# Performance work log

Hardware: AMD Instinct MI355X
Metric: run time of the kernel (lower is better)

Reference implementation:

```python
import jax, jax.numpy as jnp
import numpy as np

N_EMBED = 8192
EMBED_DIM = 64
BETA = 0.25


def setup_inputs() -> dict:
    key = jax.random.key(0)
    k_z, k_e = jax.random.split(key)
    z = jax.random.normal(k_z, (16, 4096, EMBED_DIM), dtype=jnp.float32)
    # embedding.weight.data.uniform_(-1/n_embed, 1/n_embed)
    embedding = jax.random.uniform(
        k_e, (N_EMBED, EMBED_DIM), dtype=jnp.float32,
        minval=-1.0 / N_EMBED, maxval=1.0 / N_EMBED)
    return {"z": z, "embedding": embedding}


def reference(z, embedding):
    # z: [B, H, C] with C == embed_dim (no permute needed)
    B, H, C = z.shape
    z_flat = z.reshape(-1, C)                      # [N, C]
    # squared euclidean distances: ||z||^2 + ||e||^2 - 2 z e^T
    d = (jnp.sum(z_flat ** 2, axis=1, keepdims=True)
         + jnp.sum(embedding ** 2, axis=1)
         - 2.0 * jnp.matmul(z_flat, embedding.T))  # [N, n_embed]
    idx = jnp.argmin(d, axis=1)                    # [N]
    z_q = embedding[idx].reshape(z.shape)          # gather + reshape
    sg = jax.lax.stop_gradient
    loss = (jnp.mean((sg(z_q) - z) ** 2)
            + BETA * jnp.mean((z_q - sg(z)) ** 2))
    # straight-through estimator
    z_q = z + sg(z_q - z)
    return z_q, loss, idx.reshape(B, H)
```

## Files before the change

kernel.cpp:

```cpp
#include <hip/hip_runtime.h>

typedef __attribute__((ext_vector_type(8))) short short8;
typedef __attribute__((ext_vector_type(16))) float floatx16;
typedef unsigned int u32;
typedef unsigned short u16;
typedef unsigned long long u64;

#define NROWS 65536
#define NEMB 8192
#define DIM 64
#define LOSS_OFF ((size_t)NROWS * DIM)
#define IDX_OFF (LOSS_OFF + 1)
#define CAPQ 16
#define CSTRIDE 66
#define NPREST 4

#define WS_EFRAG_OFF 0u
#define WS_BEST_OFF  (1u << 20)
#define WS_QUEUE_OFF ((1u << 20) + (512u << 10))
#define WS_LPART_OFF (WS_QUEUE_OFF + (512u << 10))
#define WS_QCNT_OFF  (WS_LPART_OFF + 8192u)
#define WS_NEED      (WS_QCNT_OFF + 64u)

__device__ __forceinline__ unsigned short f2bf(float f) {
    u32 x = __float_as_uint(f);
    return (unsigned short)((x + 0x7fffu + ((x >> 16) & 1u)) >> 16);
}

__device__ __forceinline__ float zsum_np(const float* zf) {
    float r[8];
#pragma unroll
    for (int j = 0; j < 8; ++j) r[j] = zf[j] * zf[j];
#pragma unroll
    for (int i = 8; i < 64; i += 8) {
#pragma unroll
        for (int j = 0; j < 8; ++j) r[j] += zf[i + j] * zf[i + j];
    }
    return ((r[0] + r[1]) + (r[2] + r[3])) + ((r[4] + r[5]) + (r[6] + r[7]));
}

__device__ __forceinline__ float dot_chain(const float* zf, const float* e) {
    float acc = 0.f;
#pragma unroll
    for (int i = 0; i < 16; ++i) {
        float4 ev = ((const float4*)e)[i];
        acc = fmaf(zf[4 * i + 0], ev.x, acc);
        acc = fmaf(zf[4 * i + 1], ev.y, acc);
        acc = fmaf(zf[4 * i + 2], ev.z, acc);
        acc = fmaf(zf[4 * i + 3], ev.w, acc);
    }
    return acc;
}

__device__ __forceinline__ float vmax16_3(const floatx16& a) {
    float m0 = fmaxf(fmaxf(a[0], a[1]), a[2]);
    float m1 = fmaxf(fmaxf(a[3], a[4]), a[5]);
    float m2 = fmaxf(fmaxf(a[6], a[7]), a[8]);
    float m3 = fmaxf(fmaxf(a[9], a[10]), a[11]);
    float m4 = fmaxf(fmaxf(a[12], a[13]), a[14]);
    float n0 = fmaxf(fmaxf(m0, m1), m2);
    float n1 = fmaxf(fmaxf(m3, m4), a[15]);
    return fmaxf(n0, n1);
}

__device__ __forceinline__ float fmax_h32(float x) {
#if defined(__has_builtin)
#if __has_builtin(__builtin_amdgcn_permlane32_swap)
    typedef __attribute__((ext_vector_type(2))) unsigned int uint2v;
    uint2v r = __builtin_amdgcn_permlane32_swap(
        __float_as_uint(x), __float_as_uint(x), false, false);
    return fmaxf(__uint_as_float(r[0]), __uint_as_float(r[1]));
#else
    return fmaxf(x, __shfl_xor(x, 32));
#endif
#else
    return fmaxf(x, __shfl_xor(x, 32));
#endif
}

extern "C" __global__ __launch_bounds__(256)
void vq_prep(const float* __restrict__ emb, u32* __restrict__ efrag,
             u64* __restrict__ best, u32* __restrict__ qcount) {
    int tid = blockIdx.x * 256 + threadIdx.x;
    int t = tid >> 8, kc = (tid >> 5) & 7, m = tid & 31;
    const float* e = emb + (((size_t)t * 32 + m) * 64 + kc * 8);
    float4 a = ((const float4*)e)[0];
    float4 b = ((const float4*)e)[1];
    u32 w0 = (u32)f2bf(a.x) | ((u32)f2bf(a.y) << 16);
    u32 w1 = (u32)f2bf(a.z) | ((u32)f2bf(a.w) << 16);
    u32 w2 = (u32)f2bf(b.x) | ((u32)f2bf(b.y) << 16);
    u32 w3 = (u32)f2bf(b.z) | ((u32)f2bf(b.w) << 16);
    ((uint4*)efrag)[tid] = make_uint4(w0, w1, w2, w3);
    best[tid] = ~0ull;
    if (tid < 16) qcount[tid] = 0u;
}

extern "C" __global__ __launch_bounds__(256, 4)
void vq_screen(const float* __restrict__ z, const u32* __restrict__ efrag,
               const float* __restrict__ emb, u64* __restrict__ best,
               u32* __restrict__ queue, u32* __restrict__ qcount) {
    __shared__ u16 cand[128 * CSTRIDE];
    __shared__ u32 cnt_l[512];
    __shared__ float runm_sh[128][2];
    const int tid = threadIdx.x;
    const int wave = tid >> 6, lane = tid & 63;
    const int rlo = lane & 31, h = lane >> 5;
    const int rowblk = blockIdx.x >> 1, halfid = blockIdx.x & 1;
    const int rowbase = rowblk * 128 + (wave >> 1) * 64;
    const int sub = (wave & 1) * 2 + h;
    const int wp = wave & 1;
    const int rowl0 = (wave >> 1) * 64 + rlo;
    const int rowl1 = rowl0 + 32;
    const int ebh = halfid * 4096 + wp * 64 + 4 * h;

    if (tid < 128) { runm_sh[tid][0] = -3.4e38f; runm_sh[tid][1] = -3.4e38f; }

    const u32* fb = efrag + (u32)halfid * 131072u
                  + (u32)(wp * 2048 + h * 128 + rlo * 4);

    short8 zfr[2][4];
    float eps_[2];
#pragma unroll
    for (int rt = 0; rt < 2; ++rt) {
        const float* zp = z + (size_t)(rowbase + rt * 32 + rlo) * 64;
        float sa = 0.f;
#pragma unroll
        for (int s = 0; s < 4; ++s) {
            const float4* p = (const float4*)(zp + s * 16 + h * 8);
            float4 a = p[0], b = p[1];
            union { short8 v; unsigned short e[8]; } u;
            u.e[0] = f2bf(a.x); u.e[1] = f2bf(a.y);
            u.e[2] = f2bf(a.z); u.e[3] = f2bf(a.w);
            u.e[4] = f2bf(b.x); u.e[5] = f2bf(b.y);
            u.e[6] = f2bf(b.z); u.e[7] = f2bf(b.w);
            zfr[rt][s] = u.v;
            sa += fabsf(a.x) + fabsf(a.y) + fabsf(a.z) + fabsf(a.w)
                + fabsf(b.x) + fabsf(b.y) + fabsf(b.z) + fabsf(b.w);
        }
        sa += __shfl_xor(sa, 32);
        eps_[rt] = fmaf(1.1e-6f, sa, 1e-7f);
    }
    float runm[2] = { -3.4e38f, -3.4e38f };
    u32 pc[2] = { 0u, 0u };
    const u32 cb0 = (u32)rowl0 * CSTRIDE + (u32)sub * CAPQ;
    const u32 cb1 = (u32)rowl1 * CSTRIDE + (u32)sub * CAPQ;
    const floatx16 ZACC = 0.f;

    __syncthreads();

#define PF(B_, T_, E_) do { \
    const u32* bp_ = fb + ((u32)(T_) * 4096u + (u32)(E_) * 1024u); \
    B_[0] = *(const short8*)(bp_); \
    B_[1] = *(const short8*)(bp_ + 256); \
    B_[2] = *(const short8*)(bp_ + 512); \
    B_[3] = *(const short8*)(bp_ + 768); \
} while (0)

#define TILE(B_, RT_, T_, EE_, SCAN_, CB_) do { \
    floatx16 a_ = __builtin_amdgcn_mfma_f32_32x32x16_bf16(B_[0], zfr[RT_][0], ZACC, 0, 0, 0); \
    a_ = __builtin_amdgcn_mfma_f32_32x32x16_bf16(B_[1], zfr[RT_][1], a_, 0, 0, 0); \
    a_ = __builtin_amdgcn_mfma_f32_32x32x16_bf16(B_[2], zfr[RT_][2], a_, 0, 0, 0); \
    a_ = __builtin_amdgcn_mfma_f32_32x32x16_bf16(B_[3], zfr[RT_][3], a_, 0, 0, 0); \
    float vm_ = vmax16_3(a_); \
    runm[RT_] = fmax_h32(fmaxf(runm[RT_], vm_)); \
    if (SCAN_) { \
        const float thr_ = runm[RT_] - eps_[RT_]; \
        if (vm_ >= thr_) { \
            const int ebj_ = ebh + (T_) * 128 + (EE_) * 32; \
            _Pragma("unroll") \
            for (int r_ = 0; r_ < 16; ++r_) { \
                if (a_[r_] >= thr_) { \
                    int j_ = ebj_ + ((r_ & 3) + 8 * (r_ >> 2)); \
                    if (pc[RT_] < CAPQ) cand[CB_ + pc[RT_]] = (u16)j_; \
                    pc[RT_]++;                     \
                } \
            } \
        } \
    } \
} while (0)

#define SUBSTAGE(B_, T_, EE_, SCAN_) do { \
    if (EE_ == 0) {                                \
        runm[0] = fmaxf(runm[0], runm_sh[rowl0][wp ^ 1]); \
        runm[1] = fmaxf(runm[1], runm_sh[rowl1][wp ^ 1]); \
    } \
    TILE(B_, 0, T_, EE_, SCAN_, cb0); \
    TILE(B_, 1, T_, EE_, SCAN_, cb1); \
    if (EE_ == 1 && h == 0) {                      \
        runm_sh[rowl0][wp] = runm[0]; \
        runm_sh[rowl1][wp] = runm[1]; \
    } \
} while (0)

    {
        short8 b0[4], b1[4];
        PF(b0, 0, 0);
        for (int t = 0; t < NPREST; ++t) {
            PF(b1, t, 1);
            SUBSTAGE(b0, t, 0, false);
            PF(b0, (t == NPREST - 1) ? 0 : (t + 1), 0);
            SUBSTAGE(b1, t, 1, false);
        }
        for (int t = 0; t < 32; ++t) {
            PF(b1, t, 1);
            SUBSTAGE(b0, t, 0, true);
            PF(b0, (t == 31) ? 31 : (t + 1), 0);
            SUBSTAGE(b1, t, 1, true);
        }
    }
#undef SUBSTAGE
#undef TILE
#undef PF

    cnt_l[(rowl0 << 2) + sub] = pc[0];
    cnt_l[(rowl1 << 2) + sub] = pc[1];
    __syncthreads();

    {
        const int rl = lane & 31, half = lane >> 5;
        const int rowl = wave * 32 + rl;
        const int grow = rowblk * 128 + rowl;
        const u32 ca = cnt_l[(rowl << 2) + 2 * half];
        const u32 cb = cnt_l[(rowl << 2) + 2 * half + 1];
        u32 ovf = (u32)((ca > CAPQ) | (cb > CAPQ));
        ovf |= (u32)__shfl_xor((int)ovf, 32);

        if (!ovf) {
            float zf[64];
            const float4* zp = (const float4*)(z + (size_t)grow * 64);
#pragma unroll
            for (int i = 0; i < 16; ++i) {
                float4 a = zp[i];
                zf[4 * i + 0] = a.x; zf[4 * i + 1] = a.y;
                zf[4 * i + 2] = a.z; zf[4 * i + 3] = a.w;
            }
            const float zs = zsum_np(zf);
            u64 b = ~0ull;
            const u32 cbase = (u32)rowl * CSTRIDE + (u32)(2 * half) * CAPQ;
            for (u32 s = 0; s < ca; ++s) {
                u32 j = (u32)cand[cbase + s];
                float d = fmaf(-2.f, dot_chain(zf, emb + (size_t)j * 64), zs);
                u64 p = ((u64)__float_as_uint(d) << 32) | (u64)j;
                b = p < b ? p : b;
            }
            for (u32 s = 0; s < cb; ++s) {
                u32 j = (u32)cand[cbase + CAPQ + s];
                float d = fmaf(-2.f, dot_chain(zf, emb + (size_t)j * 64), zs);
                u64 p = ((u64)__float_as_uint(d) << 32) | (u64)j;
                b = p < b ? p : b;
            }
            u64 o = __shfl_xor(b, 32);
            b = o < b ? o : b;
            if (half == 0) atomicMin(&best[grow], b);
        } else if (half == 0) {
            u32 pos = atomicAdd(qcount, 1u);
            queue[pos] = (u32)grow | ((u32)halfid << 16);
        }
    }
}

extern "C" __global__ __launch_bounds__(256)
void vq_final(const float* __restrict__ z, const float* __restrict__ emb,
              u64* __restrict__ best, const u32* __restrict__ queue,
              const u32* __restrict__ qcount, float* __restrict__ out,
              float* __restrict__ lpart) {
    __shared__ float lsum[4];
    __shared__ u64 red[4];
    const int tid = threadIdx.x, wave = tid >> 6, lane = tid & 63;

    u32 n = qcount[0]; if (n > 2u * (u32)NROWS) n = 2u * (u32)NROWS;
    for (u32 qi = 0; qi < n; ++qi) {
        const u32 e = queue[qi];
        const int row = (int)(e & 0xFFFFu);
        if ((row >> 7) != (int)blockIdx.x) continue;
        const int hb = (int)((e >> 16) & 1u) * 4096;
        const float4* zp = (const float4*)(z + (size_t)row * 64);
        float zf[64];
#pragma unroll
        for (int i = 0; i < 16; ++i) {
            float4 a = zp[i];
            zf[4 * i + 0] = a.x; zf[4 * i + 1] = a.y;
            zf[4 * i + 2] = a.z; zf[4 * i + 3] = a.w;
        }
        const float zs = zsum_np(zf);
        u64 b = ~0ull;
#pragma unroll 2
        for (int j = tid; j < 4096; j += 256) {
            const int gj = hb + j;
            float d = fmaf(-2.f, dot_chain(zf, emb + (size_t)gj * 64), zs);
            u64 p = ((u64)__float_as_uint(d) << 32) | (u64)gj;
            b = p < b ? p : b;
        }
#pragma unroll
        for (int off = 32; off; off >>= 1) {
            u64 o = __shfl_xor(b, off);
            b = o < b ? o : b;
        }
        if (lane == 0) red[wave] = b;
        __syncthreads();
        if (tid == 0) {
            u64 bb = red[0];
#pragma unroll
            for (int w = 1; w < 4; ++w) { u64 o = red[w]; bb = o < bb ? o : bb; }
            atomicMin(&best[row], bb);
        }
        __syncthreads();
    }
    __syncthreads();

    const int r2 = tid >> 1, hf = tid & 1;
    const int grow = blockIdx.x * 128 + r2;
    const u32 wj = (u32)best[grow];
    if (hf == 0) out[IDX_OFF + grow] = (float)wj;
    float lp = 0.f;
    {
        const float4* ep = (const float4*)(emb + (size_t)wj * 64) + hf * 8;
        const float4* zp4 = (const float4*)(z + (size_t)grow * 64) + hf * 8;
        float4* oq = (float4*)(out + (size_t)grow * 64) + hf * 8;
#pragma unroll
        for (int i = 0; i < 8; ++i) {
            float4 ev = ep[i];
            float4 zv = zp4[i];
            oq[i] = ev;
            float dx = ev.x - zv.x, dy = ev.y - zv.y;
            float dzv = ev.z - zv.z, dw = ev.w - zv.w;
            lp = fmaf(dx, dx, fmaf(dy, dy, fmaf(dzv, dzv, fmaf(dw, dw, lp))));
        }
    }
#pragma unroll
    for (int off = 32; off; off >>= 1) lp += __shfl_down(lp, off);
    if (lane == 0) lsum[wave] = lp;
    __syncthreads();
    if (tid == 0)
        lpart[blockIdx.x] = (lsum[0] + lsum[1]) + (lsum[2] + lsum[3]);
}

extern "C" __global__ __launch_bounds__(256)
void vq_lossred(const float* __restrict__ lpart, float* __restrict__ out) {
    __shared__ float s[256];
    const int tid = threadIdx.x;
    float v = 0.f;
    for (int i = tid; i < 512; i += 256) v += lpart[i];
    s[tid] = v; __syncthreads();
    for (int off = 128; off; off >>= 1) {
        if (tid < off) s[tid] += s[tid + off];
        __syncthreads();
    }
    if (tid == 0) out[LOSS_OFF] = 1.25f * s[0] / 4194304.f;
}

extern "C" __global__ __launch_bounds__(256, 2)
void vq_legacy(const float* __restrict__ z, const float* __restrict__ emb,
               float* __restrict__ out, float* __restrict__ ws) {
    __shared__ float tile[128 * 64];
    __shared__ float red_d[4][128];
    __shared__ int   red_i[4][128];
    const int tid = threadIdx.x, lane = tid & 63, wave = tid >> 6;
    const int r0 = blockIdx.x * 128 + lane;
    float z0f[64], z1f[64];
    {
        const float4* p0 = (const float4*)(z + (size_t)r0 * 64);
        const float4* p1 = (const float4*)(z + ((size_t)r0 + 64) * 64);
#pragma unroll
        for (int i = 0; i < 16; ++i) {
            float4 a = p0[i];
            z0f[4*i+0]=a.x; z0f[4*i+1]=a.y; z0f[4*i+2]=a.z; z0f[4*i+3]=a.w;
            float4 b = p1[i];
            z1f[4*i+0]=b.x; z1f[4*i+1]=b.y; z1f[4*i+2]=b.z; z1f[4*i+3]=b.w;
        }
    }
    const float zs0 = zsum_np(z0f), zs1 = zsum_np(z1f);
    float bd0 = 3.402823466e38f, bd1 = 3.402823466e38f;
    int bi0 = 0, bi1 = 0;
    for (int t = 0; t < 64; ++t) {
        __syncthreads();
        {
            const float4* src = (const float4*)(emb + (size_t)t * 128 * 64);
            float4* dst = (float4*)tile;
#pragma unroll
            for (int i = 0; i < 8; ++i) dst[tid + i * 256] = src[tid + i * 256];
        }
        __syncthreads();
        const int base = wave * 32;
#pragma unroll 2
        for (int jg = 0; jg < 32; jg += 4) {
            const float* e = tile + (size_t)(base + jg) * 64;
            float a00=0,a10=0,a20=0,a30=0,a01=0,a11=0,a21=0,a31=0;
#pragma unroll
            for (int i = 0; i < 16; ++i) {
                float4 ea = ((const float4*)(e))[i];
                float4 eb = ((const float4*)(e + 64))[i];
                float4 ec = ((const float4*)(e + 128))[i];
                float4 ed = ((const float4*)(e + 192))[i];
                float x0=z0f[4*i],x1=z0f[4*i+1],x2=z0f[4*i+2],x3=z0f[4*i+3];
                float y0=z1f[4*i],y1=z1f[4*i+1],y2=z1f[4*i+2],y3=z1f[4*i+3];
                a00=fmaf(x0,ea.x,a00);a00=fmaf(x1,ea.y,a00);a00=fmaf(x2,ea.z,a00);a00=fmaf(x3,ea.w,a00);
                a10=fmaf(x0,eb.x,a10);a10=fmaf(x1,eb.y,a10);a10=fmaf(x2,eb.z,a10);a10=fmaf(x3,eb.w,a10);
                a20=fmaf(x0,ec.x,a20);a20=fmaf(x1,ec.y,a20);a20=fmaf(x2,ec.z,a20);a20=fmaf(x3,ec.w,a20);
                a30=fmaf(x0,ed.x,a30);a30=fmaf(x1,ed.y,a30);a30=fmaf(x2,ed.z,a30);a30=fmaf(x3,ed.w,a30);
                a01=fmaf(y0,ea.x,a01);a01=fmaf(y1,ea.y,a01);a01=fmaf(y2,ea.z,a01);a01=fmaf(y3,ea.w,a01);
                a11=fmaf(y0,eb.x,a11);a11=fmaf(y1,eb.y,a11);a11=fmaf(y2,eb.z,a11);a11=fmaf(y3,eb.w,a11);
                a21=fmaf(y0,ec.x,a21);a21=fmaf(y1,ec.y,a21);a21=fmaf(y2,ec.z,a21);a21=fmaf(y3,ec.w,a21);
                a31=fmaf(y0,ed.x,a31);a31=fmaf(y1,ed.y,a31);a31=fmaf(y2,ed.z,a31);a31=fmaf(y3,ed.w,a31);
            }
            const int gj = t * 128 + base + jg;
            float d;
            d=fmaf(-2.f,a00,zs0); if(d<bd0){bd0=d;bi0=gj;}
            d=fmaf(-2.f,a10,zs0); if(d<bd0){bd0=d;bi0=gj+1;}
            d=fmaf(-2.f,a20,zs0); if(d<bd0){bd0=d;bi0=gj+2;}
            d=fmaf(-2.f,a30,zs0); if(d<bd0){bd0=d;bi0=gj+3;}
            d=fmaf(-2.f,a01,zs1); if(d<bd1){bd1=d;bi1=gj;}
            d=fmaf(-2.f,a11,zs1); if(d<bd1){bd1=d;bi1=gj+1;}
            d=fmaf(-2.f,a21,zs1); if(d<bd1){bd1=d;bi1=gj+2;}
            d=fmaf(-2.f,a31,zs1); if(d<bd1){bd1=d;bi1=gj+3;}
        }
    }
    red_d[wave][lane]=bd0; red_i[wave][lane]=bi0;
    red_d[wave][lane+64]=bd1; red_i[wave][lane+64]=bi1;
    __syncthreads();
    if (wave == 0) {
        float blk = 0.f;
#pragma unroll
        for (int half = 0; half < 2; ++half) {
            const int lrow = lane + half * 64;
            const float* zrf = half ? z1f : z0f;
            float bd = red_d[0][lrow]; int bi = red_i[0][lrow];
#pragma unroll
            for (int w = 1; w < 4; ++w) {
                float dd = red_d[w][lrow]; int ii = red_i[w][lrow];
                if (dd < bd || (dd == bd && ii < bi)) { bd = dd; bi = ii; }
            }
            const size_t row = (size_t)blockIdx.x * 128 + lrow;
            out[IDX_OFF + row] = (float)bi;
            const float4* ep = (const float4*)(emb + (size_t)bi * 64);
            float4* oq = (float4*)(out + row * 64);
            float ls = 0.f;
#pragma unroll
            for (int i = 0; i < 16; ++i) {
                float4 ev = ep[i];
                oq[i] = ev;
                float dx=ev.x-zrf[4*i], dy=ev.y-zrf[4*i+1];
                float dzv=ev.z-zrf[4*i+2], dw=ev.w-zrf[4*i+3];
                ls=fmaf(dx,dx,ls); ls=fmaf(dy,dy,ls); ls=fmaf(dzv,dzv,ls); ls=fmaf(dw,dw,ls);
            }
            blk += ls;
        }
#pragma unroll
        for (int off = 32; off; off >>= 1) blk += __shfl_down(blk, off);
        if (lane == 0) ws[blockIdx.x] = blk;
    }
}

extern "C" __global__ __launch_bounds__(512)
void vq_legacy_loss(const float* __restrict__ ws, float* __restrict__ out) {
    __shared__ float s[8];
    const int tid = threadIdx.x;
    float v = ws[tid];
#pragma unroll
    for (int off = 32; off; off >>= 1) v += __shfl_down(v, off);
    if ((tid & 63) == 0) s[tid >> 6] = v;
    __syncthreads();
    if (tid == 0) {
        float t = 0.f;
#pragma unroll
        for (int i = 0; i < 8; ++i) t += s[i];
        out[LOSS_OFF] = 1.25f * t / 4194304.f;
    }
}

extern "C" void kernel_launch(void* const* d_in, const int* in_sizes, int n_in,
                              void* d_out, int out_size, void* d_ws, size_t ws_size,
                              hipStream_t stream) {
    const float* z   = (const float*)d_in[0];
    const float* emb = (const float*)d_in[1];
    float* out = (float*)d_out;
    if (ws_size < (size_t)WS_NEED) {
        float* ws = (float*)d_ws;
        vq_legacy<<<512, 256, 0, stream>>>(z, emb, out, ws);
        vq_legacy_loss<<<1, 512, 0, stream>>>(ws, out);
        return;
    }
    char* wsb = (char*)d_ws;
    u32* efrag   = (u32*)(wsb + WS_EFRAG_OFF);
    u64* best    = (u64*)(wsb + WS_BEST_OFF);
    u32* queue   = (u32*)(wsb + WS_QUEUE_OFF);
    float* lpart = (float*)(wsb + WS_LPART_OFF);
    u32* qcount  = (u32*)(wsb + WS_QCNT_OFF);
    vq_prep<<<256, 256, 0, stream>>>(emb, efrag, best, qcount);
    vq_screen<<<1024, 256, 0, stream>>>(z, efrag, emb, best, queue, qcount);
    vq_final<<<512, 256, 0, stream>>>(z, emb, best, queue, qcount, out, lpart);
    vq_lossred<<<1, 256, 0, stream>>>(lpart, out);
}
```

Measured before the change: 193.6 us.

## Fuse final rescan and loss reduction into screen kernel via last-block counters

Removes the vq_final and vq_lossred launches. The second of the two screen blocks to finish a row block now does the queued fallback rescans, the gather and output writes, and the per-block loss partial. A global counter then elects the last block to reduce the loss. This saves two kernel launches and lets tail work overlap with screening in other blocks. In exchange it adds atomics and fences, and the queued rescan is serialized inside the finishing block. The shared-memory footprint of vq_screen grows, which may affect occupancy.

```diff
diff --git a/kernel.cpp b/kernel.cpp
--- a/kernel.cpp
+++ b/kernel.cpp
@@ -20,7 +20,8 @@
 #define WS_QUEUE_OFF ((1u << 20) + (512u << 10))
 #define WS_LPART_OFF (WS_QUEUE_OFF + (512u << 10))
 #define WS_QCNT_OFF  (WS_LPART_OFF + 8192u)
-#define WS_NEED      (WS_QCNT_OFF + 64u)
+#define WS_DONE_OFF  (WS_QCNT_OFF + 64u)
+#define WS_NEED      (WS_DONE_OFF + 2112u)
 
 __device__ __forceinline__ unsigned short f2bf(float f) {
     u32 x = __float_as_uint(f);
@@ -80,7 +81,8 @@
 
 extern "C" __global__ __launch_bounds__(256)
 void vq_prep(const float* __restrict__ emb, u32* __restrict__ efrag,
-             u64* __restrict__ best, u32* __restrict__ qcount) {
+             u64* __restrict__ best, u32* __restrict__ qcount,
+             u32* __restrict__ done) {
     int tid = blockIdx.x * 256 + threadIdx.x;
     int t = tid >> 8, kc = (tid >> 5) & 7, m = tid & 31;
     const float* e = emb + (((size_t)t * 32 + m) * 64 + kc * 8);
@@ -93,15 +95,22 @@
     ((uint4*)efrag)[tid] = make_uint4(w0, w1, w2, w3);
     best[tid] = ~0ull;
     if (tid < 16) qcount[tid] = 0u;
+    if (tid < 513) done[tid] = 0u;
 }
 
 extern "C" __global__ __launch_bounds__(256, 4)
 void vq_screen(const float* __restrict__ z, const u32* __restrict__ efrag,
                const float* __restrict__ emb, u64* __restrict__ best,
-               u32* __restrict__ queue, u32* __restrict__ qcount) {
+               u32* __restrict__ queue, u32* __restrict__ qcount,
+               u32* __restrict__ done, float* __restrict__ out,
+               float* __restrict__ lpart) {
     __shared__ u16 cand[128 * CSTRIDE];
     __shared__ u32 cnt_l[512];
     __shared__ float runm_sh[128][2];
+    __shared__ u64 red[4];
+    __shared__ float lsum[4];
+    __shared__ float sred[256];
+    __shared__ u32 dold;
     const int tid = threadIdx.x;
     const int wave = tid >> 6, lane = tid & 63;
     const int rlo = lane & 31, h = lane >> 5;
@@ -257,96 +266,102 @@
             queue[pos] = (u32)grow | ((u32)halfid << 16);
         }
     }
-}
-
-extern "C" __global__ __launch_bounds__(256)
-void vq_final(const float* __restrict__ z, const float* __restrict__ emb,
-              u64* __restrict__ best, const u32* __restrict__ queue,
-              const u32* __restrict__ qcount, float* __restrict__ out,
-              float* __restrict__ lpart) {
-    __shared__ float lsum[4];
-    __shared__ u64 red[4];
-    const int tid = threadIdx.x, wave = tid >> 6, lane = tid & 63;
-
-    u32 n = qcount[0]; if (n > 2u * (u32)NROWS) n = 2u * (u32)NROWS;
-    for (u32 qi = 0; qi < n; ++qi) {
-        const u32 e = queue[qi];
-        const int row = (int)(e & 0xFFFFu);
-        if ((row >> 7) != (int)blockIdx.x) continue;
-        const int hb = (int)((e >> 16) & 1u) * 4096;
-        const float4* zp = (const float4*)(z + (size_t)row * 64);
-        float zf[64];
-#pragma unroll
-        for (int i = 0; i < 16; ++i) {
-            float4 a = zp[i];
-            zf[4 * i + 0] = a.x; zf[4 * i + 1] = a.y;
-            zf[4 * i + 2] = a.z; zf[4 * i + 3] = a.w;
-        }
-        const float zs = zsum_np(zf);
-        u64 b = ~0ull;
+
+    __threadfence();
+    __syncthreads();
+    if (tid == 0) dold = atomicAdd(&done[rowblk], 1u);
+    __syncthreads();
+    if (dold == 0) return;
+    __threadfence();
+
+    {
+        u32 n = atomicAdd(qcount, 0u);
+        if (n > 2u * (u32)NROWS) n = 2u * (u32)NROWS;
+        for (u32 qi = 0; qi < n; ++qi) {
+            const u32 e = atomicAdd(&queue[qi], 0u);
+            const int row = (int)(e & 0xFFFFu);
+            if ((row >> 7) != rowblk) continue;
+            const int hb = (int)((e >> 16) & 1u) * 4096;
+            const float4* zp = (const float4*)(z + (size_t)row * 64);
+            float zf[64];
+#pragma unroll
+            for (int i = 0; i < 16; ++i) {
+                float4 a = zp[i];
+                zf[4 * i + 0] = a.x; zf[4 * i + 1] = a.y;
+                zf[4 * i + 2] = a.z; zf[4 * i + 3] = a.w;
+            }
+            const float zs = zsum_np(zf);
+            u64 b = ~0ull;
 #pragma unroll 2
-        for (int j = tid; j < 4096; j += 256) {
-            const int gj = hb + j;
-            float d = fmaf(-2.f, dot_chain(zf, emb + (size_t)gj * 64), zs);
-            u64 p = ((u64)__float_as_uint(d) << 32) | (u64)gj;
-            b = p < b ? p : b;
-        }
-#pragma unroll
-        for (int off = 32; off; off >>= 1) {
-            u64 o = __shfl_xor(b, off);
-            b = o < b ? o : b;
-        }
-        if (lane == 0) red[wave] = b;
+            for (int j = tid; j < 4096; j += 256) {
+                const int gj = hb + j;
+                float d = fmaf(-2.f, dot_chain(zf, emb + (size_t)gj * 64), zs);
+                u64 p = ((u64)__float_as_uint(d) << 32) | (u64)gj;
+                b = p < b ? p : b;
+            }
+#pragma unroll
+            for (int off = 32; off; off >>= 1) {
+                u64 o = __shfl_xor(b, off);
+                b = o < b ? o : b;
+            }
+            if (lane == 0) red[wave] = b;
+            __syncthreads();
+            if (tid == 0) {
+                u64 bb = red[0];
+#pragma unroll
+                for (int w = 1; w < 4; ++w) { u64 o = red[w]; bb = o < bb ? o : bb; }
+                atomicMin(&best[row], bb);
+            }
+            __syncthreads();
+        }
+    }
+    __syncthreads();
+
+    {
+        const int r2 = tid >> 1, hf = tid & 1;
+        const int growE = rowblk * 128 + r2;
+        const u64 bjv = atomicAdd(&best[growE], 0ull);
+        const u32 wj = (u32)bjv;
+        if (hf == 0) out[IDX_OFF + growE] = (float)wj;
+        float lp = 0.f;
+        {
+            const float4* ep = (const float4*)(emb + (size_t)wj * 64) + hf * 8;
+            const float4* zp4 = (const float4*)(z + (size_t)growE * 64) + hf * 8;
+            float4* oq = (float4*)(out + (size_t)growE * 64) + hf * 8;
+#pragma unroll
+            for (int i = 0; i < 8; ++i) {
+                float4 ev = ep[i];
+                float4 zv = zp4[i];
+                oq[i] = ev;
+                float dx = ev.x - zv.x, dy = ev.y - zv.y;
+                float dzv = ev.z - zv.z, dw = ev.w - zv.w;
+                lp = fmaf(dx, dx, fmaf(dy, dy, fmaf(dzv, dzv, fmaf(dw, dw, lp))));
+            }
+        }
+#pragma unroll
+        for (int off = 32; off; off >>= 1) lp += __shfl_down(lp, off);
+        if (lane == 0) lsum[wave] = lp;
         __syncthreads();
         if (tid == 0) {
-            u64 bb = red[0];
-#pragma unroll
-            for (int w = 1; w < 4; ++w) { u64 o = red[w]; bb = o < bb ? o : bb; }
-            atomicMin(&best[row], bb);
+            lpart[rowblk] = (lsum[0] + lsum[1]) + (lsum[2] + lsum[3]);
+            __threadfence();
+            dold = atomicAdd(&done[512], 1u);
         }
         __syncthreads();
-    }
-    __syncthreads();
-
-    const int r2 = tid >> 1, hf = tid & 1;
-    const int grow = blockIdx.x * 128 + r2;
-    const u32 wj = (u32)best[grow];
-    if (hf == 0) out[IDX_OFF + grow] = (float)wj;
-    float lp = 0.f;
+        if (dold != 511) return;
+        __threadfence();
+    }
+
     {
-        const float4* ep = (const float4*)(emb + (size_t)wj * 64) + hf * 8;
-        const float4* zp4 = (const float4*)(z + (size_t)grow * 64) + hf * 8;
-        float4* oq = (float4*)(out + (size_t)grow * 64) + hf * 8;
-#pragma unroll
-        for (int i = 0; i < 8; ++i) {
-            float4 ev = ep[i];
-            float4 zv = zp4[i];
-            oq[i] = ev;
-            float dx = ev.x - zv.x, dy = ev.y - zv.y;
-            float dzv = ev.z - zv.z, dw = ev.w - zv.w;
-            lp = fmaf(dx, dx, fmaf(dy, dy, fmaf(dzv, dzv, fmaf(dw, dw, lp))));
-        }
-    }
-#pragma unroll
-    for (int off = 32; off; off >>= 1) lp += __shfl_down(lp, off);
-    if (lane == 0) lsum[wave] = lp;
-    __syncthreads();
-    if (tid == 0)
-        lpart[blockIdx.x] = (lsum[0] + lsum[1]) + (lsum[2] + lsum[3]);
-}
-
-extern "C" __global__ __launch_bounds__(256)
-void vq_lossred(const float* __restrict__ lpart, float* __restrict__ out) {
-    __shared__ float s[256];
-    const int tid = threadIdx.x;
-    float v = 0.f;
-    for (int i = tid; i < 512; i += 256) v += lpart[i];
-    s[tid] = v; __syncthreads();
-    for (int off = 128; off; off >>= 1) {
-        if (tid < off) s[tid] += s[tid + off];
-        __syncthreads();
-    }
-    if (tid == 0) out[LOSS_OFF] = 1.25f * s[0] / 4194304.f;
+        float v = 0.f;
+        for (int i = tid; i < 512; i += 256) v += atomicAdd(&lpart[i], 0.f);
+        sred[tid] = v; __syncthreads();
+        for (int off = 128; off; off >>= 1) {
+            if (tid < off) sred[tid] += sred[tid + off];
+            __syncthreads();
+        }
+        if (tid == 0) out[LOSS_OFF] = 1.25f * sred[0] / 4194304.f;
+    }
 }
 
 extern "C" __global__ __launch_bounds__(256, 2)
@@ -486,8 +501,8 @@
     u32* queue   = (u32*)(wsb + WS_QUEUE_OFF);
     float* lpart = (float*)(wsb + WS_LPART_OFF);
     u32* qcount  = (u32*)(wsb + WS_QCNT_OFF);
-    vq_prep<<<256, 256, 0, stream>>>(emb, efrag, best, qcount);
-    vq_screen<<<1024, 256, 0, stream>>>(z, efrag, emb, best, queue, qcount);
-    vq_final<<<512, 256, 0, stream>>>(z, emb, best, queue, qcount, out, lpart);
-    vq_lossred<<<1, 256, 0, stream>>>(lpart, out);
-}
+    u32* done    = (u32*)(wsb + WS_DONE_OFF);
+    vq_prep<<<256, 256, 0, stream>>>(emb, efrag, best, qcount, done);
+    vq_screen<<<1024, 256, 0, stream>>>(z, efrag, emb, best, queue, qcount,
+                                        done, out, lpart);
+}
```

Result: slower. 422.3 us (+118.1%).
